# Performance work log

Hardware: AMD Instinct MI355X
Metric: run time of the kernel (lower is better)

## Reference

```python
import jax, jax.numpy as jnp
import numpy as np

EPS = 0.1    # entropic regularization for the approximate OT (auction-style) solve
ITERS = 20   # fixed number of Sinkhorn sweeps (mirrors fixed-iteration auction kernel)


def setup_inputs() -> dict:
    key = jax.random.key(0)
    k1, k2 = jax.random.split(key)
    pc_gen = jax.random.normal(k1, (2, 4096, 3), dtype=jnp.float32)
    pc_gt = jax.random.normal(k2, (2, 4096, 3), dtype=jnp.float32)
    return {"pc_gen": pc_gen, "pc_gt": pc_gt}


def _emd_loss(pc_gen, pc_gt):
    # Pairwise squared Euclidean cost: [B, N1, N2]
    C = jnp.sum((pc_gen[:, :, None, :] - pc_gt[:, None, :, :]) ** 2, axis=-1)
    B, N1, N2 = C.shape
    loga = -jnp.log(jnp.asarray(N1, C.dtype))  # uniform source marginal (log 1/N1)
    logb = -jnp.log(jnp.asarray(N2, C.dtype))  # uniform target marginal (log 1/N2)

    def step(carry, _):
        f, g = carry
        # log-domain Sinkhorn updates (numerically stable)
        f = EPS * (loga - jax.scipy.special.logsumexp((g[:, None, :] - C) / EPS, axis=2))
        g = EPS * (logb - jax.scipy.special.logsumexp((f[:, :, None] - C) / EPS, axis=1))
        return (f, g), None

    init = (jnp.zeros((B, N1), C.dtype), jnp.zeros((B, N2), C.dtype))
    (f, g), _ = jax.lax.scan(jax.checkpoint(step), init, None, length=ITERS)

    # Transport plan and expected matching cost per cloud.
    P = jnp.exp((f[:, :, None] + g[:, None, :] - C) / EPS)  # [B, N1, N2]
    per_cloud = jnp.sum(P * C, axis=(1, 2))  # equals (total match cost)/N1
    # Original: dist = sum of matched distances; emd_loss = (dist / N1).mean()
    return jnp.mean(per_cloud)


def reference(pc_gen, pc_gt):
    return _emd_loss(pc_gen, pc_gt)
```

## Files before the change

### kernel.cpp

```cpp
#include <hip/hip_runtime.h>


#define N   4096
#define NT  256
#define RPB 8

constexpr float EPS_F  = 0.1f;
constexpr float SHIFT  = 60.0f;
constexpr float LOG_A  = -8.317766166719343f;
constexpr float C10L   = 14.426950408889634f;
constexpr float C20L   = 28.853900817779268f;
constexpr float SHIFTL = 86.56170245333781f;
constexpr float NLN2T  = -0.06931471805599453f;
constexpr float LN2    = 0.6931471805599453f;

extern "C" __device__ float __ocml_native_exp2_f32(float);

__device__ __forceinline__ float fast_exp2(float x) {
#if __has_builtin(__builtin_amdgcn_exp2f)
    return __builtin_amdgcn_exp2f(x);
#else
    return __ocml_native_exp2_f32(x);
#endif
}

__device__ __forceinline__ float rfl(float x) {
    return __int_as_float(__builtin_amdgcn_readfirstlane(__float_as_int(x)));
}

__global__ __launch_bounds__(256) void prep_kernel(
    const float* __restrict__ gen, const float* __restrict__ gt,
    float4* __restrict__ genPack, float4* __restrict__ gtPack,
    float* __restrict__ wBaseGen, float* __restrict__ wBaseGt,
    float* __restrict__ fg, float* __restrict__ out)
{
    int t = blockIdx.x * 256 + threadIdx.x;
    int cloud = t >> 13;
    int idx   = t & 8191;
    const float* src = cloud ? gt : gen;
    float x = src[idx * 3 + 0];
    float y = src[idx * 3 + 1];
    float z = src[idx * 3 + 2];
    float nb = -C10L * fmaf(z, z, fmaf(y, y, x * x));
    (cloud ? gtPack : genPack)[idx] = make_float4(x, y, z, SHIFTL + nb);
    (cloud ? wBaseGt : wBaseGen)[idx] = nb;
    fg[t] = 0.0f;
    if (t == 0) out[0] = 0.0f;
}

__global__ __launch_bounds__(NT, 8) void sweep_kernel(
    float4*       __restrict__ packRow,
    const float4* __restrict__ packCol,
    const float*  __restrict__ wBaseRow,
    float*        __restrict__ dualRaw)
{
    const int b   = blockIdx.y;
    const int tid = threadIdx.x;
    const int rowBase = blockIdx.x * RPB;

    float4*      rp = packRow  + (size_t)b * N + rowBase;
    const float* wb = wBaseRow + (size_t)b * N + rowBase;

    float X[RPB], Y[RPB], Z[RPB], S[RPB];
    #pragma unroll
    for (int r = 0; r < RPB; ++r) {
        float4 q = rp[r];
        X[r] = rfl(q.x * C20L);
        Y[r] = rfl(q.y * C20L);
        Z[r] = rfl(q.z * C20L);
        S[r] = rfl(wb[r]);
    }

    const float4* cp = packCol + (size_t)b * N;

    float acc[RPB];
    #pragma unroll
    for (int r = 0; r < RPB; ++r) acc[r] = 0.0f;

    #pragma unroll 2
    for (int k = 0; k < N / NT; ++k) {
        float4 p = cp[tid + NT * k];
        #pragma unroll
        for (int r = 0; r < RPB; ++r) {
            float t = fmaf(Z[r], p.z, p.w);
            t = fmaf(Y[r], p.y, t);
            t = fmaf(X[r], p.x, t);
            acc[r] += fast_exp2(t + S[r]);
        }
    }

    #pragma unroll
    for (int r = 0; r < RPB; ++r) {
        float a = acc[r];
        a += __shfl_xor(a, 32);
        a += __shfl_xor(a, 16);
        a += __shfl_xor(a, 8);
        a += __shfl_xor(a, 4);
        a += __shfl_xor(a, 2);
        a += __shfl_xor(a, 1);
        acc[r] = a;
    }
    __shared__ float sred[RPB][4];
    const int wave = tid >> 6, lane = tid & 63;
    if (lane == 0) {
        #pragma unroll
        for (int r = 0; r < RPB; ++r) sred[r][wave] = acc[r];
    }
    __syncthreads();
    if (tid < RPB) {
        float s = (sred[tid][0] + sred[tid][1]) + (sred[tid][2] + sred[tid][3]);
        float dual = EPS_F * (LOG_A + SHIFT - log2f(s) * LN2);
        dualRaw[(size_t)b * N + rowBase + tid] = dual;
        ((float*)(rp + tid))[3] = fmaf(dual, C10L, SHIFTL + wb[tid]);
    }
}

__global__ __launch_bounds__(NT, 8) void loss_kernel(
    const float4* __restrict__ packGen,
    const float4* __restrict__ packGt,
    const float*  __restrict__ wBaseGen,
    const float*  __restrict__ f,
    const float*  __restrict__ g,
    float*        __restrict__ out)
{
    const int b   = blockIdx.y;
    const int tid = threadIdx.x;
    const int rowBase = blockIdx.x * RPB;

    const float4* rp = packGen  + (size_t)b * N + rowBase;
    const float*  wb = wBaseGen + (size_t)b * N + rowBase;
    const float*  fp = f        + (size_t)b * N + rowBase;

    float Ax[RPB], Ay[RPB], Az[RPB], Ri[RPB], F2[RPB];
    #pragma unroll
    for (int r = 0; r < RPB; ++r) {
        float4 q = rp[r];
        Ax[r] = rfl(q.x * -2.0f);
        Ay[r] = rfl(q.y * -2.0f);
        Az[r] = rfl(q.z * -2.0f);
        Ri[r] = rfl(wb[r] * NLN2T);
        F2[r] = rfl(fp[r] * C10L);
    }

    const float4* cp = packGt + (size_t)b * N;
    const float*  gc = g      + (size_t)b * N;

    float acc = 0.0f;
    #pragma unroll 2
    for (int k = 0; k < N / NT; ++k) {
        float4 p  = cp[tid + NT * k];
        float  gj = gc[tid + NT * k];
        float  G2 = gj * C10L;
        float  rj = fmaf(p.w - SHIFTL, NLN2T, gj);
        #pragma unroll
        for (int r = 0; r < RPB; ++r) {
            float cc = rj + Ri[r];
            cc = fmaf(Az[r], p.z, cc);
            cc = fmaf(Ay[r], p.y, cc);
            cc = fmaf(Ax[r], p.x, cc);
            float arg = fmaf(cc, -C10L, G2 + F2[r]);
            acc = fmaf(fast_exp2(arg), cc, acc);
        }
    }

    acc += __shfl_xor(acc, 32);
    acc += __shfl_xor(acc, 16);
    acc += __shfl_xor(acc, 8);
    acc += __shfl_xor(acc, 4);
    acc += __shfl_xor(acc, 2);
    acc += __shfl_xor(acc, 1);
    __shared__ float sred[4];
    const int wave = tid >> 6, lane = tid & 63;
    if (lane == 0) sred[wave] = acc;
    __syncthreads();
    if (tid == 0) {
        float t = (sred[0] + sred[1]) + (sred[2] + sred[3]);
        atomicAdd(out, t * 0.5f);
    }
}

extern "C" void kernel_launch(void* const* d_in, const int* in_sizes, int n_in,
                              void* d_out, int out_size, void* d_ws, size_t ws_size,
                              hipStream_t stream) {
    const float* gen = (const float*)d_in[0];
    const float* gt  = (const float*)d_in[1];
    float* out = (float*)d_out;

    char* ws = (char*)d_ws;
    float4* genPack  = (float4*)ws;
    float4* gtPack   = (float4*)(ws + 128 * 1024);
    float*  wBaseGen = (float*)(ws + 256 * 1024);
    float*  wBaseGt  = (float*)(ws + 288 * 1024);
    float*  f        = (float*)(ws + 320 * 1024);
    float*  g        = f + 2 * N;

    prep_kernel<<<dim3(16384 / 256), 256, 0, stream>>>(
        gen, gt, genPack, gtPack, wBaseGen, wBaseGt, f, out);

    const dim3 grid(N / RPB, 2);
    for (int it = 0; it < 20; ++it) {
        sweep_kernel<<<grid, NT, 0, stream>>>(genPack, gtPack, wBaseGen, f);
        sweep_kernel<<<grid, NT, 0, stream>>>(gtPack, genPack, wBaseGt, g);
    }
    loss_kernel<<<grid, NT, 0, stream>>>(genPack, gtPack, wBaseGen, f, g, out);
}
```

Measured before the change: 424.8 us.

## Fuse all Sinkhorn sweeps and loss into one persistent kernel with grid barriers

Replaces the 40 separate sweep launches plus the loss launch with a single kernel. Blocks synchronise between half-sweeps through a two-level atomic grid barrier, and row coordinates stay in registers across iterations. The aim is to remove per-launch overhead and the idle tail between the 41 launches. The risk is that correctness needs all 1024 blocks of 256 threads co-resident (launch bounds 4 per CU), which is assumed but never checked, and spinning on the barrier adds latency at each phase.

```diff
diff --git a/kernel.cpp b/kernel.cpp
--- a/kernel.cpp
+++ b/kernel.cpp
@@ -1,9 +1,12 @@
 #include <hip/hip_runtime.h>
 
 
-#define N   4096
-#define NT  256
-#define RPB 8
+#define N     4096
+#define NT    256
+#define RPB   8
+#define NSUB  32
+#define GRPSZ 32
+#define SUBSTRIDE 16
 
 constexpr float EPS_F  = 0.1f;
 constexpr float SHIFT  = 60.0f;
@@ -32,9 +35,11 @@
     const float* __restrict__ gen, const float* __restrict__ gt,
     float4* __restrict__ genPack, float4* __restrict__ gtPack,
     float* __restrict__ wBaseGen, float* __restrict__ wBaseGt,
-    float* __restrict__ fg, float* __restrict__ out)
+    float* __restrict__ fg, float* __restrict__ out,
+    unsigned* __restrict__ bar)
 {
     int t = blockIdx.x * 256 + threadIdx.x;
+    if (t < NSUB * SUBSTRIDE + SUBSTRIDE) bar[t] = 0u;
     int cloud = t >> 13;
     int idx   = t & 8191;
     const float* src = cloud ? gt : gen;
@@ -48,29 +53,40 @@
     if (t == 0) out[0] = 0.0f;
 }
 
-__global__ __launch_bounds__(NT, 8) void sweep_kernel(
+__device__ __forceinline__ void grid_bar(unsigned* __restrict__ bar,
+                                         int phase, int subidx)
+{
+    __syncthreads();
+    if (threadIdx.x == 0) {
+        unsigned* sub = bar + subidx * SUBSTRIDE;
+        unsigned* top = bar + NSUB * SUBSTRIDE;
+        unsigned prev = __hip_atomic_fetch_add(
+            sub, 1u, __ATOMIC_ACQ_REL, __HIP_MEMORY_SCOPE_AGENT);
+        if (prev == (unsigned)(phase + 1) * GRPSZ - 1u) {
+            __hip_atomic_fetch_add(
+                top, 1u, __ATOMIC_ACQ_REL, __HIP_MEMORY_SCOPE_AGENT);
+        }
+        unsigned ttar = (unsigned)(phase + 1) * NSUB;
+        while (__hip_atomic_load(top, __ATOMIC_RELAXED,
+                                 __HIP_MEMORY_SCOPE_AGENT) < ttar) {
+            __builtin_amdgcn_s_sleep(8);
+        }
+        __builtin_amdgcn_fence(__ATOMIC_ACQUIRE, "agent");
+    }
+    __syncthreads();
+}
+
+__device__ __forceinline__ void half_sweep(
     float4*       __restrict__ packRow,
     const float4* __restrict__ packCol,
     const float*  __restrict__ wBaseRow,
-    float*        __restrict__ dualRaw)
-{
-    const int b   = blockIdx.y;
-    const int tid = threadIdx.x;
-    const int rowBase = blockIdx.x * RPB;
-
+    float*        __restrict__ dualRaw,
+    const float (&X)[RPB], const float (&Y)[RPB],
+    const float (&Z)[RPB], const float (&S)[RPB],
+    int b, int tid, int rowBase, float (&sred)[RPB][4])
+{
     float4*      rp = packRow  + (size_t)b * N + rowBase;
     const float* wb = wBaseRow + (size_t)b * N + rowBase;
-
-    float X[RPB], Y[RPB], Z[RPB], S[RPB];
-    #pragma unroll
-    for (int r = 0; r < RPB; ++r) {
-        float4 q = rp[r];
-        X[r] = rfl(q.x * C20L);
-        Y[r] = rfl(q.y * C20L);
-        Z[r] = rfl(q.z * C20L);
-        S[r] = rfl(wb[r]);
-    }
-
     const float4* cp = packCol + (size_t)b * N;
 
     float acc[RPB];
@@ -100,7 +116,6 @@
         a += __shfl_xor(a, 1);
         acc[r] = a;
     }
-    __shared__ float sred[RPB][4];
     const int wave = tid >> 6, lane = tid & 63;
     if (lane == 0) {
         #pragma unroll
@@ -115,67 +130,102 @@
     }
 }
 
-__global__ __launch_bounds__(NT, 8) void loss_kernel(
-    const float4* __restrict__ packGen,
-    const float4* __restrict__ packGt,
-    const float*  __restrict__ wBaseGen,
-    const float*  __restrict__ f,
-    const float*  __restrict__ g,
-    float*        __restrict__ out)
-{
-    const int b   = blockIdx.y;
-    const int tid = threadIdx.x;
+__global__ __launch_bounds__(NT, 4) void sinkhorn_main(
+    float4* __restrict__ genPack, float4* __restrict__ gtPack,
+    const float* __restrict__ wBaseGen, const float* __restrict__ wBaseGt,
+    float* __restrict__ f, float* __restrict__ g,
+    unsigned* __restrict__ bar, float* __restrict__ out)
+{
+    const int b       = blockIdx.y;
+    const int tid     = threadIdx.x;
     const int rowBase = blockIdx.x * RPB;
-
-    const float4* rp = packGen  + (size_t)b * N + rowBase;
-    const float*  wb = wBaseGen + (size_t)b * N + rowBase;
-    const float*  fp = f        + (size_t)b * N + rowBase;
-
-    float Ax[RPB], Ay[RPB], Az[RPB], Ri[RPB], F2[RPB];
+    const int bid     = b * (N / RPB) + blockIdx.x;
+    const int subidx  = bid >> 5;
+    __shared__ float sred[RPB][4];
+
+    const float4* rpG = genPack  + (size_t)b * N + rowBase;
+    const float4* rpT = gtPack   + (size_t)b * N + rowBase;
+    const float*  wbG = wBaseGen + (size_t)b * N + rowBase;
+    const float*  wbT = wBaseGt  + (size_t)b * N + rowBase;
+
+    float XG[RPB], YG[RPB], ZG[RPB], SG[RPB];
+    float XT[RPB], YT[RPB], ZT[RPB], ST[RPB];
     #pragma unroll
     for (int r = 0; r < RPB; ++r) {
-        float4 q = rp[r];
-        Ax[r] = rfl(q.x * -2.0f);
-        Ay[r] = rfl(q.y * -2.0f);
-        Az[r] = rfl(q.z * -2.0f);
-        Ri[r] = rfl(wb[r] * NLN2T);
-        F2[r] = rfl(fp[r] * C10L);
-    }
-
-    const float4* cp = packGt + (size_t)b * N;
-    const float*  gc = g      + (size_t)b * N;
-
-    float acc = 0.0f;
-    #pragma unroll 2
-    for (int k = 0; k < N / NT; ++k) {
-        float4 p  = cp[tid + NT * k];
-        float  gj = gc[tid + NT * k];
-        float  G2 = gj * C10L;
-        float  rj = fmaf(p.w - SHIFTL, NLN2T, gj);
+        float4 q = rpG[r];
+        XG[r] = rfl(q.x * C20L);
+        YG[r] = rfl(q.y * C20L);
+        ZG[r] = rfl(q.z * C20L);
+        SG[r] = rfl(wbG[r]);
+    }
+    #pragma unroll
+    for (int r = 0; r < RPB; ++r) {
+        float4 q = rpT[r];
+        XT[r] = rfl(q.x * C20L);
+        YT[r] = rfl(q.y * C20L);
+        ZT[r] = rfl(q.z * C20L);
+        ST[r] = rfl(wbT[r]);
+    }
+
+    int phase = 0;
+    #pragma unroll 1
+    for (int it = 0; it < 20; ++it) {
+        half_sweep(genPack, gtPack, wBaseGen, f,
+                   XG, YG, ZG, SG, b, tid, rowBase, sred);
+        grid_bar(bar, phase++, subidx);
+        half_sweep(gtPack, genPack, wBaseGt, g,
+                   XT, YT, ZT, ST, b, tid, rowBase, sred);
+        grid_bar(bar, phase++, subidx);
+    }
+
+    {
+        const float* fp = f + (size_t)b * N + rowBase;
+
+        float Ax[RPB], Ay[RPB], Az[RPB], Ri[RPB], F2[RPB];
         #pragma unroll
         for (int r = 0; r < RPB; ++r) {
-            float cc = rj + Ri[r];
-            cc = fmaf(Az[r], p.z, cc);
-            cc = fmaf(Ay[r], p.y, cc);
-            cc = fmaf(Ax[r], p.x, cc);
-            float arg = fmaf(cc, -C10L, G2 + F2[r]);
-            acc = fmaf(fast_exp2(arg), cc, acc);
-        }
-    }
-
-    acc += __shfl_xor(acc, 32);
-    acc += __shfl_xor(acc, 16);
-    acc += __shfl_xor(acc, 8);
-    acc += __shfl_xor(acc, 4);
-    acc += __shfl_xor(acc, 2);
-    acc += __shfl_xor(acc, 1);
-    __shared__ float sred[4];
-    const int wave = tid >> 6, lane = tid & 63;
-    if (lane == 0) sred[wave] = acc;
-    __syncthreads();
-    if (tid == 0) {
-        float t = (sred[0] + sred[1]) + (sred[2] + sred[3]);
-        atomicAdd(out, t * 0.5f);
+            float4 q = rpG[r];
+            Ax[r] = rfl(q.x * -2.0f);
+            Ay[r] = rfl(q.y * -2.0f);
+            Az[r] = rfl(q.z * -2.0f);
+            Ri[r] = rfl(wbG[r] * NLN2T);
+            F2[r] = rfl(fp[r] * C10L);
+        }
+
+        const float4* cp = gtPack + (size_t)b * N;
+        const float*  gc = g      + (size_t)b * N;
+
+        float acc = 0.0f;
+        #pragma unroll 2
+        for (int k = 0; k < N / NT; ++k) {
+            float4 p  = cp[tid + NT * k];
+            float  gj = gc[tid + NT * k];
+            float  G2 = gj * C10L;
+            float  rj = fmaf(p.w - SHIFTL, NLN2T, gj);
+            #pragma unroll
+            for (int r = 0; r < RPB; ++r) {
+                float cc = rj + Ri[r];
+                cc = fmaf(Az[r], p.z, cc);
+                cc = fmaf(Ay[r], p.y, cc);
+                cc = fmaf(Ax[r], p.x, cc);
+                float arg = fmaf(cc, -C10L, G2 + F2[r]);
+                acc = fmaf(fast_exp2(arg), cc, acc);
+            }
+        }
+
+        acc += __shfl_xor(acc, 32);
+        acc += __shfl_xor(acc, 16);
+        acc += __shfl_xor(acc, 8);
+        acc += __shfl_xor(acc, 4);
+        acc += __shfl_xor(acc, 2);
+        acc += __shfl_xor(acc, 1);
+        const int wave = tid >> 6, lane = tid & 63;
+        if (lane == 0) sred[0][wave] = acc;
+        __syncthreads();
+        if (tid == 0) {
+            float t2 = (sred[0][0] + sred[0][1]) + (sred[0][2] + sred[0][3]);
+            atomicAdd(out, t2 * 0.5f);
+        }
     }
 }
 
@@ -187,20 +237,17 @@
     float* out = (float*)d_out;
 
     char* ws = (char*)d_ws;
-    float4* genPack  = (float4*)ws;
-    float4* gtPack   = (float4*)(ws + 128 * 1024);
-    float*  wBaseGen = (float*)(ws + 256 * 1024);
-    float*  wBaseGt  = (float*)(ws + 288 * 1024);
-    float*  f        = (float*)(ws + 320 * 1024);
-    float*  g        = f + 2 * N;
+    float4*   genPack  = (float4*)ws;
+    float4*   gtPack   = (float4*)(ws + 128 * 1024);
+    float*    wBaseGen = (float*)(ws + 256 * 1024);
+    float*    wBaseGt  = (float*)(ws + 288 * 1024);
+    float*    f        = (float*)(ws + 320 * 1024);
+    float*    g        = f + 2 * N;
+    unsigned* bar      = (unsigned*)(ws + 384 * 1024);
 
     prep_kernel<<<dim3(16384 / 256), 256, 0, stream>>>(
-        gen, gt, genPack, gtPack, wBaseGen, wBaseGt, f, out);
-
-    const dim3 grid(N / RPB, 2);
-    for (int it = 0; it < 20; ++it) {
-        sweep_kernel<<<grid, NT, 0, stream>>>(genPack, gtPack, wBaseGen, f);
-        sweep_kernel<<<grid, NT, 0, stream>>>(gtPack, genPack, wBaseGt, g);
-    }
-    loss_kernel<<<grid, NT, 0, stream>>>(genPack, gtPack, wBaseGen, f, g, out);
-}
+        gen, gt, genPack, gtPack, wBaseGen, wBaseGt, f, out, bar);
+
+    sinkhorn_main<<<dim3(N / RPB, 2), NT, 0, stream>>>(
+        genPack, gtPack, wBaseGen, wBaseGt, f, g, bar, out);
+}
```

Result: slower. 1.555 ms (+266.1%).
